# Optimization experiments

Measured on AMD Instinct MI355X. Metric: run time of the kernel, lower is better.

The kernel has to match this reference:

```python
import jax, jax.numpy as jnp
import numpy as np
from jax import lax

B, T, C = 4, 2048, 2048
HK, HV = 16, 16
DK, DV = 128, 128
KW = 4  # conv kernel width
KEY_DIM = HK * DK      # 2048
VAL_DIM = HV * DV      # 2048
QKV_DIM = 2 * KEY_DIM + VAL_DIM  # 6144
EPS_RMS = 1e-6
EPS_NORM = 1e-12


def setup_inputs() -> dict:
    key = jax.random.key(0)
    ks = jax.random.split(key, 7)
    s = 0.02
    x = jax.random.normal(ks[0], (B, T, C), dtype=jnp.float32)
    positions = jnp.broadcast_to(jnp.arange(T, dtype=jnp.int64 if jax.config.jax_enable_x64 else jnp.int32), (B, T))
    W_qkvz = jax.random.normal(ks[1], (C, QKV_DIM + VAL_DIM), dtype=jnp.float32) * s
    W_b = jax.random.normal(ks[2], (C, HV), dtype=jnp.float32) * s
    W_a = jax.random.normal(ks[3], (C, HV), dtype=jnp.float32) * s
    conv_w = jax.random.normal(ks[4], (QKV_DIM, 1, KW), dtype=jnp.float32) * 0.1
    norm_w = jnp.ones((DV,), dtype=jnp.float32)
    W_out = jax.random.normal(ks[5], (VAL_DIM, C), dtype=jnp.float32) * s
    return {"x": x, "positions": positions, "W_qkvz": W_qkvz, "W_b": W_b,
            "W_a": W_a, "conv_w": conv_w, "norm_w": norm_w, "W_out": W_out}


def _l2norm(u):
    n = jnp.sqrt(jnp.sum(u * u, axis=-1, keepdims=True))
    return u / jnp.maximum(n, EPS_NORM)


def _forward(x, W_qkvz, W_b, W_a, conv_w, norm_w, W_out):
    qkvz = x @ W_qkvz                               # [B,T,QKV+VAL]
    qkv, z = qkvz[..., :QKV_DIM], qkvz[..., QKV_DIM:]
    z = z.reshape(B, T, HV, DV)
    beta = jax.nn.sigmoid(x @ W_b)                  # [B,T,HV]
    alpha = jax.nn.sigmoid(x @ W_a)                 # [B,T,HV]

    # depthwise causal conv1d (padding K-1 then truncate to T)
    xc = jnp.transpose(qkv, (0, 2, 1))              # [B,QKV_DIM,T]
    xc = lax.conv_general_dilated(xc, conv_w, window_strides=(1,),
                                  padding=[(KW - 1, 0)],
                                  feature_group_count=QKV_DIM,
                                  dimension_numbers=("NCH", "OIH", "NCH"))
    qkv = jnp.transpose(jax.nn.silu(xc), (0, 2, 1))  # [B,T,QKV_DIM]

    q = _l2norm(qkv[..., :KEY_DIM].reshape(B, T, HK, DK))
    k = _l2norm(qkv[..., KEY_DIM:2 * KEY_DIM].reshape(B, T, HK, DK))
    v = qkv[..., 2 * KEY_DIM:].reshape(B, T, HV, DV)

    def step(state, inp):
        q_t, k_t, v_t, b_t, a_t = inp               # [B,H,DK],[B,H,DK],[B,H,DV],[B,H],[B,H]
        state = a_t[:, :, None, None] * state + \
                b_t[:, :, None, None] * (k_t[..., :, None] * v_t[:, :, None, :])
        out = jnp.einsum('bhk,bhkv->bhv', q_t, state)
        return state, out

    state0 = jnp.zeros((B, HK, DK, DV), dtype=x.dtype)
    seq = (jnp.moveaxis(q, 1, 0), jnp.moveaxis(k, 1, 0), jnp.moveaxis(v, 1, 0),
           jnp.moveaxis(beta, 1, 0), jnp.moveaxis(alpha, 1, 0))
    _, outs = lax.scan(step, state0, seq)           # [T,B,H,DV]
    out = jnp.moveaxis(outs, 0, 1)                  # [B,T,H,DV]

    # RMSNorm over head_v_dim (fp32), gated by sigmoid(z)
    of = out.astype(jnp.float32)
    rms = jnp.mean(of * of, axis=-1, keepdims=True)
    out = ((of * lax.rsqrt(rms + EPS_RMS)) * norm_w).astype(out.dtype)
    out = out * jax.nn.sigmoid(z)
    return out.reshape(B, T, VAL_DIM) @ W_out


def reference(x, positions, W_qkvz, W_b, W_a, conv_w, norm_w, W_out):
    return _forward(x, W_qkvz, W_b, W_a, conv_w, norm_w, W_out)
```

## Files before the change

### kernel.cpp

```cpp
#include <hip/hip_runtime.h>
#include <hip/hip_bf16.h>

typedef __bf16 bf16_t;
typedef __attribute__((ext_vector_type(8))) __bf16 bf16x8;
typedef __attribute__((ext_vector_type(4))) float floatx4;


__device__ __forceinline__ void gload16(const void* g, void* l) {
  __builtin_amdgcn_global_load_lds(
      (const __attribute__((address_space(1))) void*)g,
      (__attribute__((address_space(3))) void*)l, 16, 0, 0);
}

__global__ void k_transpose_cast(const float* __restrict__ in, bf16_t* __restrict__ out,
                                 int R, int Ccols) {
  __shared__ float tile[32][33];
  int c0 = blockIdx.x * 32, r0 = blockIdx.y * 32;
  for (int i = threadIdx.y; i < 32; i += 8)
    tile[i][threadIdx.x] = in[(long)(r0 + i) * Ccols + c0 + threadIdx.x];
  __syncthreads();
  for (int i = threadIdx.y; i < 32; i += 8)
    out[(long)(c0 + i) * R + r0 + threadIdx.x] = (bf16_t)tile[threadIdx.x][i];
}

__global__ void k_transpose_f32(const float* __restrict__ in, float* __restrict__ out,
                                int R, int Ccols) {
  int r = blockIdx.x * blockDim.x + threadIdx.x;
  if (r < R)
    for (int c = 0; c < Ccols; ++c) out[(long)c * R + r] = in[(long)r * Ccols + c];
}

__global__ __launch_bounds__(256) void k_beta_alpha(const float* __restrict__ x,
                                                    const float* __restrict__ WbT,
                                                    const float* __restrict__ WaT,
                                                    float* __restrict__ beta,
                                                    float* __restrict__ alpha,
                                                    bf16_t* __restrict__ xb) {
  extern __shared__ float xs[];
  const long row0 = (long)blockIdx.x * 16;
  const int tid = threadIdx.x;
  {
    const float4* src = (const float4*)(x + row0 * 2048);
    float4* dst = (float4*)xs;
    for (int i = tid; i < 16 * 512; i += 256) dst[i] = src[i];
  }
  __syncthreads();
  {
    bf16_t* xbrow = xb + row0 * 2048;
    for (int i = tid; i < 4096; i += 256) {
      const float4 a = *(const float4*)&xs[i * 8];
      const float4 b2 = *(const float4*)&xs[i * 8 + 4];
      bf16x8 o;
      o[0] = (bf16_t)a.x; o[1] = (bf16_t)a.y; o[2] = (bf16_t)a.z; o[3] = (bf16_t)a.w;
      o[4] = (bf16_t)b2.x; o[5] = (bf16_t)b2.y; o[6] = (bf16_t)b2.z; o[7] = (bf16_t)b2.w;
      *(bf16x8*)(xbrow + i * 8) = o;
    }
  }
  const int wv = tid >> 6, lane = tid & 63;
  for (int oo = 0; oo < 8; ++oo) {
    const int o = wv * 8 + oo;
    const float* Wrow = (o < 16) ? (WbT + (long)o * 2048) : (WaT + (long)(o - 16) * 2048);
    float acc[16];
#pragma unroll
    for (int r = 0; r < 16; ++r) acc[r] = 0.f;
    for (int kc = 0; kc < 8; ++kc) {
      const float4 w4 = *(const float4*)(Wrow + kc * 256 + lane * 4);
#pragma unroll
      for (int r = 0; r < 16; ++r) {
        const float4 xv = *(const float4*)&xs[r * 2048 + kc * 256 + lane * 4];
        acc[r] += w4.x * xv.x + w4.y * xv.y + w4.z * xv.z + w4.w * xv.w;
      }
    }
#pragma unroll
    for (int r = 0; r < 16; ++r) {
      float s = acc[r];
      for (int off = 32; off; off >>= 1) s += __shfl_down(s, off);
      if (lane == 0) {
        const long row = row0 + r;
        const int b = (int)(row >> 11), t = (int)(row & 2047);
        const float sig = 1.f / (1.f + __expf(-s));
        float* dst = (o < 16) ? beta : alpha;
        dst[((long)(b * 16 + (o & 15))) * 2048 + t] = sig;
      }
    }
  }
}

template <typename OUT_T>
__global__ __launch_bounds__(512, 2) void k_gemm256(const bf16_t* __restrict__ A,
                                                    const bf16_t* __restrict__ Bt,
                                                    OUT_T* __restrict__ C,
                                                    int N, int K, int lda) {
  extern __shared__ char gsm[];
  const int m0 = blockIdx.y * 256, n0 = blockIdx.x * 256;
  const int tid = threadIdx.x;
  const int w = tid >> 6, l = tid & 63;
  const int wm = w >> 2, wn = w & 3;
  const int l15 = l & 15, lg = l >> 4;

  const bf16_t* asrc[4];
  const bf16_t* bsrc[4];
  int dofs[4];
#pragma unroll
  for (int t = 0; t < 4; ++t) {
    int c = t * 512 + tid;
    int row = c >> 3, cs = (c & 7) ^ (row & 7);
    asrc[t] = A + (long)(m0 + row) * lda + cs * 8;
    bsrc[t] = Bt + (long)(n0 + row) * K + cs * 8;
    dofs[t] = c * 16;
  }

  auto STAGE = [&](int buf, int k0) {
    char* ab = gsm + buf * 65536;
    char* bb = ab + 32768;
#pragma unroll
    for (int t = 0; t < 4; ++t) {
      gload16(asrc[t] + k0, ab + dofs[t]);
      gload16(bsrc[t] + k0, bb + dofs[t]);
    }
  };

  floatx4 acc[8][4] = {};
  STAGE(0, 0);
  const int NK = K >> 6;
  for (int kt = 0; kt < NK; ++kt) {
    __syncthreads();
    if (kt + 1 < NK) STAGE((kt + 1) & 1, (kt + 1) << 6);
    const char* As_ = gsm + (kt & 1) * 65536;
    const char* Bs_ = As_ + 32768;
#pragma unroll
    for (int ks = 0; ks < 2; ++ks) {
      bf16x8 af[8], bfr[4];
#pragma unroll
      for (int mi = 0; mi < 8; ++mi) {
        const int r = wm * 128 + mi * 16 + l15;
        af[mi] = *(const bf16x8*)(As_ + r * 128 + ((((ks << 2) + lg) ^ (r & 7)) << 4));
      }
#pragma unroll
      for (int ni = 0; ni < 4; ++ni) {
        const int r = wn * 64 + ni * 16 + l15;
        bfr[ni] = *(const bf16x8*)(Bs_ + r * 128 + ((((ks << 2) + lg) ^ (r & 7)) << 4));
      }
      __builtin_amdgcn_s_setprio(1);
#pragma unroll
      for (int mi = 0; mi < 8; ++mi)
#pragma unroll
        for (int ni = 0; ni < 4; ++ni)
          acc[mi][ni] = __builtin_amdgcn_mfma_f32_16x16x32_bf16(af[mi], bfr[ni], acc[mi][ni], 0, 0, 0);
      __builtin_amdgcn_s_setprio(0);
    }
  }
  const int crow0 = m0 + wm * 128 + lg * 4;
  const int ccol = n0 + wn * 64 + l15;
#pragma unroll
  for (int mi = 0; mi < 8; ++mi)
#pragma unroll
    for (int ni = 0; ni < 4; ++ni)
#pragma unroll
      for (int r = 0; r < 4; ++r)
        C[(long)(crow0 + mi * 16 + r) * N + ccol + ni * 16] = (OUT_T)acc[mi][ni][r];
}

__global__ __launch_bounds__(256) void k_conv(const bf16_t* __restrict__ qkvz,
                                              const float* __restrict__ conv_w,
                                              bf16_t* __restrict__ q, bf16_t* __restrict__ k,
                                              bf16_t* __restrict__ v) {
  int row = blockIdx.x;
  int b = row >> 11, t = row & 2047;
  __shared__ float ys[6144];
  __shared__ float gsum[32][9];
  __shared__ float norms[32];
  const int c0 = threadIdx.x * 8;
  for (int c8 = c0; c8 < 6144; c8 += 2048) {
    bf16x8 xr[4];
#pragma unroll
    for (int w2 = 0; w2 < 4; ++w2) {
      int tt = t - 3 + w2;
      bf16x8 zr = {};
      xr[w2] = (tt >= 0) ? *(const bf16x8*)&qkvz[((long)(b * 2048 + tt)) * 8192 + c8] : zr;
    }
#pragma unroll
    for (int j = 0; j < 8; ++j) {
      float4 wv = *(const float4*)&conv_w[(c8 + j) * 4];
      float a = (float)xr[0][j] * wv.x + (float)xr[1][j] * wv.y +
                (float)xr[2][j] * wv.z + (float)xr[3][j] * wv.w;
      ys[c8 + j] = a / (1.f + __expf(-a));
    }
  }
  __syncthreads();
  {
    int g = threadIdx.x >> 3, j = threadIdx.x & 7;
    float s = 0.f;
#pragma unroll
    for (int e = 0; e < 16; ++e) {
      float yv = ys[g * 128 + j * 16 + e];
      s += yv * yv;
    }
    gsum[g][j] = s;
  }
  __syncthreads();
  if (threadIdx.x < 32) {
    float s = 0.f;
#pragma unroll
    for (int j = 0; j < 8; j++) s += gsum[threadIdx.x][j];
    norms[threadIdx.x] = 1.f / fmaxf(sqrtf(s), 1e-12f);
  }
  __syncthreads();
  for (int c8 = c0; c8 < 6144; c8 += 2048) {
    float scale;
    bf16_t* dst;
    if (c8 < 2048) {
      int h = c8 >> 7;
      scale = norms[h];
      dst = q + (((long)(b * 16 + h)) * 2048 + t) * 128 + (c8 & 127);
    } else if (c8 < 4096) {
      int h = (c8 - 2048) >> 7;
      scale = norms[16 + h];
      dst = k + (((long)(b * 16 + h)) * 2048 + t) * 128 + (c8 & 127);
    } else {
      scale = 1.f;
      int h = (c8 - 4096) >> 7;
      dst = v + (((long)(b * 16 + h)) * 2048 + t) * 128 + (c8 & 127);
    }
    bf16x8 o;
#pragma unroll
    for (int j = 0; j < 8; ++j) o[j] = (bf16_t)(ys[c8 + j] * scale);
    *(bf16x8*)dst = o;
  }
}

__global__ __launch_bounds__(256) void k_tr_kv(const bf16_t* __restrict__ kv,
                                               const bf16_t* __restrict__ vv,
                                               bf16_t* __restrict__ qkvz) {
  __shared__ bf16_t t_lds[64 * 136];
  int bh = blockIdx.x >> 5, tc = blockIdx.x & 31;
  int t0 = tc * 64;
  int tid = threadIdx.x;
#pragma unroll
  for (int pass = 0; pass < 2; ++pass) {
    const bf16_t* src = (pass == 0 ? kv : vv) + (long)bh * 2048 * 128 + (long)t0 * 128;
    int r = tid >> 2, sc = (tid & 3) * 32;
    bf16x8 x0 = *(const bf16x8*)(src + (long)r * 128 + sc);
    bf16x8 x1 = *(const bf16x8*)(src + (long)r * 128 + sc + 8);
    bf16x8 x2 = *(const bf16x8*)(src + (long)r * 128 + sc + 16);
    bf16x8 x3 = *(const bf16x8*)(src + (long)r * 128 + sc + 24);
    __syncthreads();
    *(bf16x8*)&t_lds[r * 136 + sc] = x0;
    *(bf16x8*)&t_lds[r * 136 + sc + 8] = x1;
    *(bf16x8*)&t_lds[r * 136 + sc + 16] = x2;
    *(bf16x8*)&t_lds[r * 136 + sc + 24] = x3;
    __syncthreads();
    int d = tid >> 1, h2 = tid & 1;
    bf16_t* dst = qkvz + (long)(bh * 128 + d) * 8192 + (pass ? 4096 : 2048) + t0 + h2 * 32;
#pragma unroll
    for (int g = 0; g < 4; ++g) {
      bf16x8 o;
#pragma unroll
      for (int j = 0; j < 8; ++j) o[j] = t_lds[(h2 * 32 + g * 8 + j) * 136 + d];
      *(bf16x8*)(dst + g * 8) = o;
    }
  }
}

__global__ __launch_bounds__(512, 1) void k_scan_chunked(
    const bf16_t* __restrict__ qv, const bf16_t* __restrict__ kv,
    bf16_t* __restrict__ qkvz, float* __restrict__ so_hi,
    const float* __restrict__ beta, const float* __restrict__ alpha) {
  extern __shared__ char smem[];
  bf16_t* q_lds = (bf16_t*)smem;
  bf16_t* kn_lds = q_lds + 8704;
  bf16_t* kT_lds = kn_lds + 8704;
  bf16_t* vT_lds = kT_lds + 9216;
  bf16_t* P_lds = vT_lds + 2304;
  bf16_t* St_lds = P_lds + 4608;
  float* G_lds = (float*)(St_lds + 4352);
  float* bet_lds = G_lds + 64;
  float* w_lds = bet_lds + 64;
  float* eG_lds = w_lds + 64;

  const int bh = blockIdx.x, dvb = blockIdx.y;
  const int b = bh >> 4, h = bh & 15;
  const int tid = threadIdx.x;
  const int w = tid >> 6, l = tid & 63;
  const int l15 = l & 15, lg = l >> 4;
  const int g = w & 1, r = w >> 1;

  const bf16_t* qb = qv + (long)bh * 2048 * 128;
  const bf16_t* kb = kv + (long)bh * 2048 * 128;
  const bf16_t* kTg = qkvz + (long)bh * 128 * 8192 + 2048;
  const bf16_t* vTg = qkvz + (long)(bh * 128 + dvb * 32) * 8192 + 4096;
  const float* bet = beta + (long)bh * 2048;
  const float* alp = alpha + (long)bh * 2048;

  floatx4 streg[2] = {};
  for (int i = tid; i < 2176; i += 512) ((float*)St_lds)[i] = 0.f;
  __syncthreads();

  const int sr = tid >> 3, ssc = (tid & 7) * 16;
  const int sdk = tid >> 2, ssc2 = (tid & 3) * 16;
  const int svr = tid >> 3, svc = (tid & 7) * 8;

  bf16x8 ra0, ra1, rb0, rb1, rc0, rc1, rd0 = {};
  float rbet = 0.f, ralp = 1.f;
  {
    const bf16_t* qs = qb + (long)sr * 128 + ssc;
    const bf16_t* ks = kb + (long)sr * 128 + ssc;
    const bf16_t* kts = kTg + (long)sdk * 8192 + ssc2;
    ra0 = *(const bf16x8*)qs; ra1 = *(const bf16x8*)(qs + 8);
    rb0 = *(const bf16x8*)ks; rb1 = *(const bf16x8*)(ks + 8);
    rc0 = *(const bf16x8*)kts; rc1 = *(const bf16x8*)(kts + 8);
    if (tid < 256) rd0 = *(const bf16x8*)(vTg + (long)svr * 8192 + svc);
    if (w == 0) { rbet = bet[l]; ralp = alp[l]; }
  }

  for (int c = 0; c < 32; ++c) {
    const int t0 = c * 64;
    {
      *(bf16x8*)&q_lds[sr * 136 + ssc] = ra0;
      *(bf16x8*)&q_lds[sr * 136 + ssc + 8] = ra1;
      *(bf16x8*)&kn_lds[sr * 136 + ssc] = rb0;
      *(bf16x8*)&kn_lds[sr * 136 + ssc + 8] = rb1;
      *(bf16x8*)&kT_lds[sdk * 72 + ssc2] = rc0;
      *(bf16x8*)&kT_lds[sdk * 72 + ssc2 + 8] = rc1;
      if (tid < 256) *(bf16x8*)&vT_lds[svr * 72 + svc] = rd0;
      if (w == 0) {
        float bsv = rbet;
        float la = __logf(ralp);
#pragma unroll
        for (int off = 1; off < 64; off <<= 1) {
          float xup = __shfl_up(la, off);
          if (l >= off) la += xup;
        }
        float ge = __shfl(la, 63);
        G_lds[l] = la;
        bet_lds[l] = bsv;
        w_lds[l] = bsv * __expf(ge - la);
        eG_lds[l] = __expf(la);
      }
    }
    __syncthreads();

    if (c + 1 < 32) {
      const int t1 = t0 + 64;
      const bf16_t* qs = qb + (long)(t1 + sr) * 128 + ssc;
      const bf16_t* ks = kb + (long)(t1 + sr) * 128 + ssc;
      const bf16_t* kts = kTg + (long)sdk * 8192 + t1 + ssc2;
      ra0 = *(const bf16x8*)qs; ra1 = *(const bf16x8*)(qs + 8);
      rb0 = *(const bf16x8*)ks; rb1 = *(const bf16x8*)(ks + 8);
      rc0 = *(const bf16x8*)kts; rc1 = *(const bf16x8*)(kts + 8);
      if (tid < 256) rd0 = *(const bf16x8*)(vTg + (long)svr * 8192 + t1 + svc);
      if (w == 0) { rbet = bet[t1 + l]; ralp = alp[t1 + l]; }
    }

    {
      bf16_t* p = &kT_lds[sdk * 72 + ssc2];
      bf16x8 x0 = *(bf16x8*)p, x1 = *(bf16x8*)(p + 8);
#pragma unroll
      for (int j = 0; j < 8; j++) {
        x0[j] = (bf16_t)((float)x0[j] * w_lds[ssc2 + j]);
        x1[j] = (bf16_t)((float)x1[j] * w_lds[ssc2 + 8 + j]);
      }
      *(bf16x8*)p = x0;
      *(bf16x8*)(p + 8) = x1;
    }

    {
      const int mi = w >> 1;
      bf16x8 aq[4];
#pragma unroll
      for (int ks = 0; ks < 4; ks++)
        aq[ks] = *(bf16x8*)&q_lds[(mi * 16 + l15) * 136 + ks * 32 + lg * 8];
#pragma unroll
      for (int sn2 = 0; sn2 < 2; sn2++) {
        const int sn = (w & 1) * 2 + sn2;
        floatx4 sc_ = {0.f, 0.f, 0.f, 0.f};
#pragma unroll
        for (int ks = 0; ks < 4; ks++) {
          bf16x8 bk = *(bf16x8*)&kn_lds[(sn * 16 + l15) * 136 + ks * 32 + lg * 8];
          sc_ = __builtin_amdgcn_mfma_f32_16x16x32_bf16(aq[ks], bk, sc_, 0, 0, 0);
        }
        const int sl = sn * 16 + l15;
        const float gs = G_lds[sl], bs = bet_lds[sl];
#pragma unroll
        for (int rr = 0; rr < 4; rr++) {
          const int tl = mi * 16 + lg * 4 + rr;
          float val = (sl <= tl) ? sc_[rr] * __expf(G_lds[tl] - gs) * bs : 0.f;
          P_lds[tl * 72 + sl] = (bf16_t)val;
        }
      }
    }
    __syncthreads();

    floatx4 acco = {0.f, 0.f, 0.f, 0.f};
    {
      const int rloc = g * 16 + l15;
      bf16x8 av0 = *(bf16x8*)&vT_lds[rloc * 72 + lg * 8];
      bf16x8 av1 = *(bf16x8*)&vT_lds[rloc * 72 + 32 + lg * 8];
      floatx4 f = {0.f, 0.f, 0.f, 0.f};
#pragma unroll
      for (int ks = 0; ks < 4; ks++) {
        bf16x8 aq = *(bf16x8*)&q_lds[(r * 16 + l15) * 136 + ks * 32 + lg * 8];
        bf16x8 bs_ = *(bf16x8*)&St_lds[rloc * 136 + ks * 32 + lg * 8];
        f = __builtin_amdgcn_mfma_f32_16x16x32_bf16(aq, bs_, f, 0, 0, 0);
      }
#pragma unroll
      for (int rr = 0; rr < 4; rr++) f[rr] *= eG_lds[r * 16 + lg * 4 + rr];
#pragma unroll
      for (int ks2 = 0; ks2 < 2; ks2++) {
        bf16x8 ap = *(bf16x8*)&P_lds[(r * 16 + l15) * 72 + ks2 * 32 + lg * 8];
        f = __builtin_amdgcn_mfma_f32_16x16x32_bf16(ap, (ks2 == 0) ? av0 : av1, f, 0, 0, 0);
      }
      acco = f;
      const float dcv = eG_lds[63];
#pragma unroll
      for (int ni = 0; ni < 2; ni++) {
        const int ni2 = r * 2 + ni;
#pragma unroll
        for (int rr = 0; rr < 4; rr++) streg[ni][rr] *= dcv;
        bf16x8 bk0 = *(bf16x8*)&kT_lds[(ni2 * 16 + l15) * 72 + lg * 8];
        bf16x8 bk1 = *(bf16x8*)&kT_lds[(ni2 * 16 + l15) * 72 + 32 + lg * 8];
        streg[ni] = __builtin_amdgcn_mfma_f32_16x16x32_bf16(av0, bk0, streg[ni], 0, 0, 0);
        streg[ni] = __builtin_amdgcn_mfma_f32_16x16x32_bf16(av1, bk1, streg[ni], 0, 0, 0);
      }
    }
    __syncthreads();

#pragma unroll
    for (int ni = 0; ni < 2; ni++) {
      const int ni2 = r * 2 + ni;
#pragma unroll
      for (int rr = 0; rr < 4; rr++)
        St_lds[(g * 16 + lg * 4 + rr) * 136 + ni2 * 16 + l15] = (bf16_t)streg[ni][rr];
    }
    {
      const int dvg = dvb * 32 + g * 16 + l15;
      const int hcol = h * 128 + dvg;
#pragma unroll
      for (int rr = 0; rr < 4; rr++) {
        const int t = t0 + r * 16 + lg * 4 + rr;
        const long row = (long)b * 2048 + t;
        if (hcol < 1024)
          ((float*)qkvz)[row * 4096 + hcol] = acco[rr];
        else
          so_hi[row * 1024 + hcol - 1024] = acco[rr];
      }
    }
  }
}

__global__ __launch_bounds__(256) void k_rmsgate(const float* __restrict__ so_hi,
                                                 const bf16_t* __restrict__ qkvz,
                                                 bf16_t* __restrict__ A2,
                                                 const float* __restrict__ norm_w) {
  long row = blockIdx.x;
  int tid = threadIdx.x;
  int h = tid >> 4, j = tid & 15;
  const float* srow = (h < 8) ? (const float*)qkvz + row * 4096 + h * 128 + j * 8
                              : so_hi + row * 1024 + (h - 8) * 128 + j * 8;
  float xv[8];
  *(float4*)&xv[0] = *(const float4*)srow;
  *(float4*)&xv[4] = *(const float4*)(srow + 4);
  float ss = 0.f;
#pragma unroll
  for (int e = 0; e < 8; e++) ss += xv[e] * xv[e];
  ss += __shfl_xor(ss, 1); ss += __shfl_xor(ss, 2);
  ss += __shfl_xor(ss, 4); ss += __shfl_xor(ss, 8);
  float rinv = rsqrtf(ss * (1.0f / 128.0f) + 1e-6f);
  const bf16_t* zrow = qkvz + row * 8192 + 6144 + h * 128 + j * 8;
  bf16x8 zv = *(const bf16x8*)zrow;
  bf16x8 o;
#pragma unroll
  for (int e = 0; e < 8; e++) {
    float z = (float)zv[e];
    float gate = 1.f / (1.f + __expf(-z));
    o[e] = (bf16_t)(xv[e] * rinv * norm_w[j * 8 + e] * gate);
  }
  *(bf16x8*)(A2 + row * 2048 + h * 128 + j * 8) = o;
}

extern "C" void kernel_launch(void* const* d_in, const int* in_sizes, int n_in,
                              void* d_out, int out_size, void* d_ws, size_t ws_size,
                              hipStream_t stream) {
  const float* x      = (const float*)d_in[0];
  const float* W_qkvz = (const float*)d_in[2];
  const float* W_b    = (const float*)d_in[3];
  const float* W_a    = (const float*)d_in[4];
  const float* conv_w = (const float*)d_in[5];
  const float* norm_w = (const float*)d_in[6];
  const float* W_out  = (const float*)d_in[7];
  float* out = (float*)d_out;
  char* ws = (char*)d_ws;

  bf16_t* qkvz  = (bf16_t*)(ws + 0);
  bf16_t* xb    = (bf16_t*)(ws + 134217728);
  bf16_t* qv    = (bf16_t*)(ws + 134217728);
  bf16_t* A2    = (bf16_t*)(ws + 134217728);
  bf16_t* WqT   = (bf16_t*)(ws + 167772160);
  bf16_t* kv    = (bf16_t*)(ws + 167772160);
  bf16_t* vv    = (bf16_t*)(ws + 201326592);
  float*  so_hi = (float*)(ws + 201326592);
  bf16_t* WoT   = (bf16_t*)(ws + 234881024);
  float*  WbT   = (float*)(ws + 243269632);
  float*  WaT   = (float*)(ws + 243400704);
  float*  beta  = (float*)(ws + 243531776);
  float*  alpha = (float*)(ws + 244056064);

  if (ws_size < 244580352) return;

  k_transpose_cast<<<dim3(8192 / 32, 2048 / 32), dim3(32, 8), 0, stream>>>(W_qkvz, WqT, 2048, 8192);
  k_transpose_cast<<<dim3(2048 / 32, 2048 / 32), dim3(32, 8), 0, stream>>>(W_out, WoT, 2048, 2048);
  k_transpose_f32<<<8, 256, 0, stream>>>(W_b, WbT, 2048, 16);
  k_transpose_f32<<<8, 256, 0, stream>>>(W_a, WaT, 2048, 16);
  k_beta_alpha<<<512, 256, 131072, stream>>>(x, WbT, WaT, beta, alpha, xb);
  k_gemm256<bf16_t><<<dim3(32, 32), 512, 131072, stream>>>(xb, WqT, qkvz, 8192, 2048, 2048);
  k_conv<<<8192, 256, 0, stream>>>(qkvz, conv_w, qv, kv, vv);
  k_tr_kv<<<2048, 256, 0, stream>>>(kv, vv, qkvz);
  k_scan_chunked<<<dim3(64, 4), 512, 76800, stream>>>(qv, kv, qkvz, so_hi, beta, alpha);
  k_rmsgate<<<8192, 256, 0, stream>>>(so_hi, qkvz, A2, norm_w);
  k_gemm256<float><<<dim3(8, 32), 512, 131072, stream>>>(A2, WoT, out, 2048, 2048, 2048);
  (void)in_sizes; (void)n_in; (void)out_size;
}
```

Baseline: 821.8 us.

## Pipeline GEMM loads in half-K-tile stages with vmcnt-based waits

Restructures the 256x256 bf16 GEMM main loop so each 64-wide K tile is split into two 32-wide halves stored in separate LDS regions, with a new swizzle for the 64-byte rows. Global-to-LDS loads are issued in four phases interleaved with the MFMA work, keeping up to two K-steps in flight, and full __syncthreads is replaced by s_waitcnt vmcnt plus raw barriers. The goal is to overlap memory latency with compute at finer grain and reduce sync stalls. The cost is more barriers per tile and fragile hand-written waitcnt counts; the tail clamps the prefetch index, so redundant loads are issued on the last iterations.

```diff
diff --git a/kernel.cpp b/kernel.cpp
--- a/kernel.cpp
+++ b/kernel.cpp
@@ -98,56 +98,68 @@
   const int wm = w >> 2, wn = w & 3;
   const int l15 = l & 15, lg = l >> 4;
 
-  const bf16_t* asrc[4];
-  const bf16_t* bsrc[4];
-  int dofs[4];
-#pragma unroll
-  for (int t = 0; t < 4; ++t) {
+  const bf16_t* aRow[2];
+  const bf16_t* bRow[2];
+  int dofs[2];
+#pragma unroll
+  for (int t = 0; t < 2; ++t) {
     int c = t * 512 + tid;
-    int row = c >> 3, cs = (c & 7) ^ (row & 7);
-    asrc[t] = A + (long)(m0 + row) * lda + cs * 8;
-    bsrc[t] = Bt + (long)(n0 + row) * K + cs * 8;
+    int row = c >> 2;
+    int cs = (c & 3) ^ ((row >> 1) & 3);
+    aRow[t] = A + (long)(m0 + row) * lda + cs * 8;
+    bRow[t] = Bt + (long)(n0 + row) * K + cs * 8;
     dofs[t] = c * 16;
   }
-
-  auto STAGE = [&](int buf, int k0) {
-    char* ab = gsm + buf * 65536;
-    char* bb = ab + 32768;
-#pragma unroll
-    for (int t = 0; t < 4; ++t) {
-      gload16(asrc[t] + k0, ab + dofs[t]);
-      gload16(bsrc[t] + k0, bb + dofs[t]);
-    }
+  const int NK = K >> 6;
+
+  auto STAGE = [&](int buf, int isB, int h, int jj) {
+    char* base = gsm + buf * 65536 + isB * 32768 + h * 16384;
+    const int kofs = jj * 64 + h * 32;
+#pragma unroll
+    for (int t = 0; t < 2; ++t)
+      gload16((isB ? bRow[t] : aRow[t]) + kofs, base + dofs[t]);
   };
 
   floatx4 acc[8][4] = {};
-  STAGE(0, 0);
-  const int NK = K >> 6;
-  for (int kt = 0; kt < NK; ++kt) {
-    __syncthreads();
-    if (kt + 1 < NK) STAGE((kt + 1) & 1, (kt + 1) << 6);
-    const char* As_ = gsm + (kt & 1) * 65536;
-    const char* Bs_ = As_ + 32768;
-#pragma unroll
-    for (int ks = 0; ks < 2; ++ks) {
-      bf16x8 af[8], bfr[4];
-#pragma unroll
-      for (int mi = 0; mi < 8; ++mi) {
-        const int r = wm * 128 + mi * 16 + l15;
-        af[mi] = *(const bf16x8*)(As_ + r * 128 + ((((ks << 2) + lg) ^ (r & 7)) << 4));
+  const int j1 = (NK > 1) ? 1 : 0;
+  STAGE(0, 0, 0, 0); STAGE(0, 1, 0, 0); STAGE(0, 0, 1, 0); STAGE(0, 1, 1, 0);
+  STAGE(1, 0, 0, j1); STAGE(1, 1, 0, j1);
+
+  for (int j = 0; j < NK; ++j) {
+    const int buf = j & 1;
+    const int jn1 = (j + 1 < NK) ? j + 1 : NK - 1;
+    const int jn2 = (j + 2 < NK) ? j + 2 : NK - 1;
+#pragma unroll
+    for (int p = 0; p < 4; ++p) {
+      const int ks = p >> 1, m = p & 1;
+      if (m == 0) asm volatile("s_waitcnt vmcnt(8)" ::: "memory");
+      __builtin_amdgcn_s_barrier();
+      const char* Ar = gsm + buf * 65536 + ks * 16384;
+      const char* Br = Ar + 32768;
+      bf16x8 af[4], bfr[4];
+#pragma unroll
+      for (int mi = 0; mi < 4; ++mi) {
+        const int r = wm * 128 + (m * 4 + mi) * 16 + l15;
+        af[mi] = *(const bf16x8*)(Ar + r * 64 + ((lg ^ ((r >> 1) & 3)) << 4));
       }
 #pragma unroll
       for (int ni = 0; ni < 4; ++ni) {
         const int r = wn * 64 + ni * 16 + l15;
-        bfr[ni] = *(const bf16x8*)(Bs_ + r * 128 + ((((ks << 2) + lg) ^ (r & 7)) << 4));
-      }
+        bfr[ni] = *(const bf16x8*)(Br + r * 64 + ((lg ^ ((r >> 1) & 3)) << 4));
+      }
+      if (p == 0)      STAGE(buf ^ 1, 0, 1, jn1);
+      else if (p == 1) STAGE(buf ^ 1, 1, 1, jn1);
+      else if (p == 2) STAGE(buf, 0, 0, jn2);
+      else             STAGE(buf, 1, 0, jn2);
       __builtin_amdgcn_s_setprio(1);
 #pragma unroll
-      for (int mi = 0; mi < 8; ++mi)
+      for (int mi = 0; mi < 4; ++mi)
 #pragma unroll
         for (int ni = 0; ni < 4; ++ni)
-          acc[mi][ni] = __builtin_amdgcn_mfma_f32_16x16x32_bf16(af[mi], bfr[ni], acc[mi][ni], 0, 0, 0);
+          acc[m * 4 + mi][ni] =
+              __builtin_amdgcn_mfma_f32_16x16x32_bf16(af[mi], bfr[ni], acc[m * 4 + mi][ni], 0, 0, 0);
       __builtin_amdgcn_s_setprio(0);
+      asm volatile("s_waitcnt lgkmcnt(0)" ::: "memory");
     }
   }
   const int crow0 = m0 + wm * 128 + lg * 4;
```

Result: slower. 852.2 us (+3.7%).
